# Optimization experiments

Hardware: AMD Instinct MI355X
Metric: run time of the kernel (lower is better)

## Reference

```python
import jax, jax.numpy as jnp
import numpy as np
from jax import lax

T, B, V, N = 128, 256, 256, 1024


def setup_inputs() -> dict:
    key = jax.random.key(0)
    k1, k2, k3, k4 = jax.random.split(key, 4)
    inputs = jax.random.uniform(k1, (T, B, V), dtype=jnp.float32)
    labels = jax.random.uniform(k2, (T * B, V), dtype=jnp.float32)
    weights = jax.random.normal(k3, (V + N, N), dtype=jnp.float32) * 0.1
    bias = jnp.zeros((N,), dtype=jnp.float32)
    output_weights = jax.random.normal(k4, (N, V), dtype=jnp.float32) * 0.1
    output_bias = jnp.zeros((V,), dtype=jnp.float32)
    return {
        "inputs": inputs,
        "labels": labels,
        "weights": weights,
        "bias": bias,
        "output_weights": output_weights,
        "output_bias": output_bias,
    }


def reference(inputs, labels, weights, bias, output_weights, output_bias):
    t, b, v = inputs.shape
    n = weights.shape[1]
    # split concat-matmul into x@Wx + h@Wh (same math as concat([x,h]) @ W)
    w_x = weights[:v]   # [V, N]
    w_h = weights[v:]   # [N, N]

    def step(h, x):
        h_new = jnp.tanh(x @ w_x + h @ w_h + bias)
        return h_new, h_new

    h0 = jnp.zeros((b, n), dtype=inputs.dtype)
    _, outputs = lax.scan(step, h0, inputs)          # [T, B, N]
    outputs = outputs.reshape(t * b, n)              # concat over time
    logits = outputs @ output_weights + output_bias  # [T*B, V]
    # softmax_cross_entropy_with_logits (soft labels), then mean
    log_p = jax.nn.log_softmax(logits, axis=-1)
    loss = jnp.mean(-jnp.sum(labels * log_p, axis=-1))
    return loss
```

## Files before the change

### kernel.cpp

```cpp
#include <hip/hip_runtime.h>
#include <math.h>

typedef __bf16 bf16;
typedef __attribute__((ext_vector_type(4))) __bf16 bf16x4;
typedef __attribute__((ext_vector_type(8))) __bf16 bf16x8;
typedef __attribute__((ext_vector_type(4))) float f32x4;

#define T_STEPS 128
#define B_SZ    256
#define V_SZ    256
#define N_SZ    1024
#define NROWS   (T_STEPS * B_SZ)
#define RSTR    68
#define LSTR    17
#define NGRP    16
#define NCB     16

__device__ __forceinline__ float fast_tanh(float x) {
    float e = __expf(2.0f * x);
    return 1.0f - 2.0f / (e + 1.0f);
}

__device__ __forceinline__ bf16x8 cvt_bf16x8(float4 a, float4 b) {
    bf16x8 r;
    r[0] = (bf16)a.x; r[1] = (bf16)a.y; r[2] = (bf16)a.z; r[3] = (bf16)a.w;
    r[4] = (bf16)b.x; r[5] = (bf16)b.y; r[6] = (bf16)b.z; r[7] = (bf16)b.w;
    return r;
}

__global__ __launch_bounds__(256) void k_prep(
    const float* __restrict__ weights,
    const float* __restrict__ out_w,
    bf16* __restrict__ Wxt,
    bf16* __restrict__ Wht,
    bf16* __restrict__ Wot)
{
    __shared__ float tile[32][33];
    int id = blockIdx.x;
    const float* src; bf16* dst; int R, C, tr, tc;
    if (id < 256) {
        src = weights; dst = Wxt; R = V_SZ; C = N_SZ;
        tr = (id & 7) * 32; tc = (id >> 3) * 32;
    } else if (id < 1280) {
        id -= 256;
        src = weights + (size_t)V_SZ * N_SZ; dst = Wht; R = N_SZ; C = N_SZ;
        tr = (id & 31) * 32; tc = (id >> 5) * 32;
    } else {
        id -= 1280;
        src = out_w; dst = Wot; R = N_SZ; C = V_SZ;
        tr = (id & 31) * 32; tc = (id >> 5) * 32;
    }
    int tx = threadIdx.x & 31;
    int ty = threadIdx.x >> 5;
#pragma unroll
    for (int i = 0; i < 32; i += 8)
        tile[ty + i][tx] = src[(size_t)(tr + ty + i) * C + tc + tx];
    __syncthreads();
#pragma unroll
    for (int i = 0; i < 32; i += 8)
        dst[(size_t)(tc + ty + i) * R + tr + tx] = (bf16)tile[tx][ty + i];
}

__global__ __launch_bounds__(512, 2) void k_rnn(
    const float* __restrict__ Xf,
    const bf16* __restrict__ Wxt,
    const bf16* __restrict__ Wht,
    const bf16* __restrict__ Wot,
    const float* __restrict__ bias,
    bf16* __restrict__ XH,
    unsigned int* __restrict__ Lgu,
    int* __restrict__ cnt)
{
    __shared__ float red[8 * 16 * RSTR];
    __shared__ float lred[8 * 16 * LSTR];
    const int tid  = threadIdx.x;
    const int lane = tid & 63;
    const int w    = tid >> 6;
    const int quad = lane >> 4;
    const int l15  = lane & 15;
    const int g  = blockIdx.x >> 4;
    const int c  = blockIdx.x & 15;
    const int m0 = g * 16;
    const int n0 = c * 64;
    const int k0 = w * 128;
    const int v0 = w * 32;
    int* gcnt = cnt + g * T_STEPS;

    const bf16* Bp = Wht + (size_t)(n0 + l15) * N_SZ + k0 + quad * 8;
    bf16x8 b[4][4];
#pragma unroll
    for (int nt = 0; nt < 4; ++nt)
#pragma unroll
        for (int kc = 0; kc < 4; ++kc)
            b[nt][kc] = *(const bf16x8*)&Bp[(size_t)(nt * 16) * N_SZ + kc * 32];
    bf16x8 bx[4];
#pragma unroll
    for (int nt = 0; nt < 4; ++nt)
        bx[nt] = *(const bf16x8*)&Wxt[(size_t)(n0 + nt * 16 + l15) * V_SZ + v0 + quad * 8];
    bf16x8 bo[4];
#pragma unroll
    for (int kc = 0; kc < 4; ++kc)
        bo[kc] = *(const bf16x8*)&Wot[(size_t)(c * 16 + l15) * N_SZ + k0 + kc * 32 + quad * 8];

    const int orow = tid >> 5;
    const int ocol = (tid & 31) * 2;
    const float bias0 = bias[n0 + ocol];
    const float bias1 = bias[n0 + ocol + 1];
    const int lrow = w * 2 + (lane >> 3);
    const int lvp  = lane & 7;
    unsigned int* XHu = (unsigned int*)XH;
    const f32x4 zz = {0.f, 0.f, 0.f, 0.f};
    const size_t xin = (size_t)(m0 + l15) * V_SZ + v0 + quad * 8;

    {
        float4 f0 = *(const float4*)&Xf[xin];
        float4 f1 = *(const float4*)&Xf[xin + 4];
        bf16x8 ax = cvt_bf16x8(f0, f1);
        f32x4 acc[4] = {zz, zz, zz, zz};
#pragma unroll
        for (int nt = 0; nt < 4; ++nt)
            acc[nt] = __builtin_amdgcn_mfma_f32_16x16x32_bf16(ax, bx[nt], acc[nt], 0, 0, 0);
#pragma unroll
        for (int nt = 0; nt < 4; ++nt)
#pragma unroll
            for (int r = 0; r < 4; ++r)
                red[(w * 16 + quad * 4 + r) * RSTR + nt * 16 + l15] = acc[nt][r];
        __syncthreads();
        float s0 = bias0, s1 = bias1;
#pragma unroll
        for (int w2 = 0; w2 < 8; ++w2) {
            float2 v = *(const float2*)&red[(w2 * 16 + orow) * RSTR + ocol];
            s0 += v.x; s1 += v.y;
        }
        bf16 r0 = (bf16)fast_tanh(s0);
        bf16 r1 = (bf16)fast_tanh(s1);
        unsigned int outw = (unsigned int)__builtin_bit_cast(unsigned short, r0)
                          | ((unsigned int)__builtin_bit_cast(unsigned short, r1) << 16);
        size_t oidx = (((size_t)m0 + orow) * N_SZ + n0 + ocol) >> 1;
        __hip_atomic_store(&XHu[oidx], outw, __ATOMIC_RELAXED, __HIP_MEMORY_SCOPE_AGENT);
        asm volatile("s_waitcnt vmcnt(0)" ::: "memory");
        __syncthreads();
        if (tid == 0)
            __hip_atomic_fetch_add(&gcnt[0], 1, __ATOMIC_RELAXED, __HIP_MEMORY_SCOPE_AGENT);
    }

    for (int t = 1; t < T_STEPS; ++t) {
        float4 f0 = *(const float4*)&Xf[(size_t)t * B_SZ * V_SZ + xin];
        float4 f1 = *(const float4*)&Xf[(size_t)t * B_SZ * V_SZ + xin + 4];

        if (tid == 0) {
            while (__hip_atomic_load(&gcnt[t - 1], __ATOMIC_RELAXED,
                                     __HIP_MEMORY_SCOPE_AGENT) < NCB)
                __builtin_amdgcn_s_sleep(1);
        }
        __syncthreads();

        const bf16* Ap = XH + ((size_t)(t - 1) * B_SZ + m0 + l15) * N_SZ + k0 + quad * 8;
        bf16x8 a[4];
#pragma unroll
        for (int kc = 0; kc < 4; ++kc)
            a[kc] = *(const bf16x8*)&Ap[kc * 32];

        bf16x8 ax = cvt_bf16x8(f0, f1);
        f32x4 acc[4] = {zz, zz, zz, zz};
#pragma unroll
        for (int nt = 0; nt < 4; ++nt)
            acc[nt] = __builtin_amdgcn_mfma_f32_16x16x32_bf16(ax, bx[nt], acc[nt], 0, 0, 0);
#pragma unroll
        for (int kc = 0; kc < 4; ++kc)
#pragma unroll
            for (int nt = 0; nt < 4; ++nt)
                acc[nt] = __builtin_amdgcn_mfma_f32_16x16x32_bf16(a[kc], b[nt][kc],
                                                                  acc[nt], 0, 0, 0);
        f32x4 lacc = zz;
#pragma unroll
        for (int kc = 0; kc < 4; ++kc)
            lacc = __builtin_amdgcn_mfma_f32_16x16x32_bf16(a[kc], bo[kc], lacc, 0, 0, 0);

#pragma unroll
        for (int nt = 0; nt < 4; ++nt)
#pragma unroll
            for (int r = 0; r < 4; ++r)
                red[(w * 16 + quad * 4 + r) * RSTR + nt * 16 + l15] = acc[nt][r];
#pragma unroll
        for (int r = 0; r < 4; ++r)
            lred[(w * 16 + quad * 4 + r) * LSTR + l15] = lacc[r];
        __syncthreads();

        float s0 = bias0, s1 = bias1;
#pragma unroll
        for (int w2 = 0; w2 < 8; ++w2) {
            float2 v = *(const float2*)&red[(w2 * 16 + orow) * RSTR + ocol];
            s0 += v.x; s1 += v.y;
        }
        bf16 r0 = (bf16)fast_tanh(s0);
        bf16 r1 = (bf16)fast_tanh(s1);
        unsigned int outw = (unsigned int)__builtin_bit_cast(unsigned short, r0)
                          | ((unsigned int)__builtin_bit_cast(unsigned short, r1) << 16);
        size_t oidx = (((size_t)t * B_SZ + m0 + orow) * N_SZ + n0 + ocol) >> 1;
        __hip_atomic_store(&XHu[oidx], outw, __ATOMIC_RELAXED, __HIP_MEMORY_SCOPE_AGENT);

        if (lane < 16) {
            float sa = 0.f, sb = 0.f;
#pragma unroll
            for (int w2 = 0; w2 < 8; ++w2) {
                sa += lred[(w2 * 16 + lrow) * LSTR + lvp * 2];
                sb += lred[(w2 * 16 + lrow) * LSTR + lvp * 2 + 1];
            }
            bf16 pa = (bf16)sa, pb = (bf16)sb;
            unsigned int pw = (unsigned int)__builtin_bit_cast(unsigned short, pa)
                            | ((unsigned int)__builtin_bit_cast(unsigned short, pb) << 16);
            Lgu[(((size_t)(t - 1) * 16 + c) * B_SZ + m0 + lrow) * 8 + lvp] = pw;
        }

        asm volatile("s_waitcnt vmcnt(0)" ::: "memory");
        __syncthreads();
        if (tid == 0)
            __hip_atomic_fetch_add(&gcnt[t], 1, __ATOMIC_RELAXED, __HIP_MEMORY_SCOPE_AGENT);
    }

    if (tid == 0) {
        while (__hip_atomic_load(&gcnt[T_STEPS - 1], __ATOMIC_RELAXED,
                                 __HIP_MEMORY_SCOPE_AGENT) < NCB)
            __builtin_amdgcn_s_sleep(1);
    }
    __syncthreads();
    {
        const bf16* Ap = XH + ((size_t)(T_STEPS - 1) * B_SZ + m0 + l15) * N_SZ + k0 + quad * 8;
        bf16x8 a[4];
#pragma unroll
        for (int kc = 0; kc < 4; ++kc)
            a[kc] = *(const bf16x8*)&Ap[kc * 32];
        f32x4 lacc = zz;
#pragma unroll
        for (int kc = 0; kc < 4; ++kc)
            lacc = __builtin_amdgcn_mfma_f32_16x16x32_bf16(a[kc], bo[kc], lacc, 0, 0, 0);
#pragma unroll
        for (int r = 0; r < 4; ++r)
            lred[(w * 16 + quad * 4 + r) * LSTR + l15] = lacc[r];
        __syncthreads();
        if (lane < 16) {
            float sa = 0.f, sb = 0.f;
#pragma unroll
            for (int w2 = 0; w2 < 8; ++w2) {
                sa += lred[(w2 * 16 + lrow) * LSTR + lvp * 2];
                sb += lred[(w2 * 16 + lrow) * LSTR + lvp * 2 + 1];
            }
            bf16 pa = (bf16)sa, pb = (bf16)sb;
            unsigned int pw = (unsigned int)__builtin_bit_cast(unsigned short, pa)
                            | ((unsigned int)__builtin_bit_cast(unsigned short, pb) << 16);
            Lgu[(((size_t)(T_STEPS - 1) * 16 + c) * B_SZ + m0 + lrow) * 8 + lvp] = pw;
        }
    }
}

__global__ __launch_bounds__(256) void k_lred(
    const bf16* __restrict__ Lg,
    const float* __restrict__ labels,
    const float* __restrict__ ob,
    float* __restrict__ out)
{
    __shared__ float bt[4];
    const int tid  = threadIdx.x;
    const int lane = tid & 63;
    const int w    = tid >> 6;
    const int cs   = lane >> 2;
    const int vi   = (lane & 3) * 4;
    const float4 ob4 = *(const float4*)&ob[cs * 16 + vi];

    float wtot = 0.f;
    for (int i = 0; i < 32; ++i) {
        int row  = blockIdx.x * 128 + w * 32 + i;
        int p    = row >> 8;
        int brow = row & 255;
        bf16x4 lv = *(const bf16x4*)&Lg[(((size_t)p * 16 + cs) * B_SZ + brow) * 16 + vi];
        float l0 = (float)lv.x + ob4.x;
        float l1 = (float)lv.y + ob4.y;
        float l2 = (float)lv.z + ob4.z;
        float l3 = (float)lv.w + ob4.w;
        float mx = fmaxf(fmaxf(l0, l1), fmaxf(l2, l3));
#pragma unroll
        for (int sft = 1; sft < 64; sft <<= 1)
            mx = fmaxf(mx, __shfl_xor(mx, sft, 64));
        float sume = __expf(l0 - mx) + __expf(l1 - mx) + __expf(l2 - mx) + __expf(l3 - mx);
        const float4 lb = *(const float4*)&labels[(size_t)row * V_SZ + cs * 16 + vi];
        float labs = lb.x + lb.y + lb.z + lb.w;
        float labv = lb.x * l0 + lb.y * l1 + lb.z * l2 + lb.w * l3;
#pragma unroll
        for (int sft = 1; sft < 64; sft <<= 1) {
            sume += __shfl_xor(sume, sft, 64);
            labs += __shfl_xor(labs, sft, 64);
            labv += __shfl_xor(labv, sft, 64);
        }
        float lse = mx + __logf(sume);
        wtot += labs * lse - labv;
    }
    if (lane == 0) bt[w] = wtot;
    __syncthreads();
    if (tid == 0)
        atomicAdd(out, (bt[0] + bt[1] + bt[2] + bt[3]) * (1.0f / (float)NROWS));
}

extern "C" void kernel_launch(void* const* d_in, const int* in_sizes, int n_in,
                              void* d_out, int out_size, void* d_ws, size_t ws_size,
                              hipStream_t stream)
{
    const float* inputs  = (const float*)d_in[0];
    const float* labels  = (const float*)d_in[1];
    const float* weights = (const float*)d_in[2];
    const float* bias    = (const float*)d_in[3];
    const float* out_w   = (const float*)d_in[4];
    const float* out_b   = (const float*)d_in[5];
    float* out = (float*)d_out;

    char* ws = (char*)d_ws;
    bf16* XH  = (bf16*)ws;  ws += (size_t)NROWS * N_SZ * 2;
    bf16* Lg  = (bf16*)ws;  ws += (size_t)NROWS * V_SZ * 2;
    bf16* Wxt = (bf16*)ws;  ws += (size_t)N_SZ * V_SZ * 2;
    bf16* Wht = (bf16*)ws;  ws += (size_t)N_SZ * N_SZ * 2;
    bf16* Wot = (bf16*)ws;  ws += (size_t)V_SZ * N_SZ * 2;
    int*  cnt = (int*)ws;   ws += (size_t)NGRP * T_STEPS * 4;

    hipMemsetAsync(out, 0, sizeof(float), stream);
    hipMemsetAsync(cnt, 0, (size_t)NGRP * T_STEPS * 4, stream);

    k_prep<<<dim3(1536), 256, 0, stream>>>(weights, out_w, Wxt, Wht, Wot);

    k_rnn<<<dim3(NGRP * NCB), 512, 0, stream>>>(inputs, Wxt, Wht, Wot, bias, XH,
                                                (unsigned int*)Lg, cnt);

    k_lred<<<dim3(NROWS / 128), 256, 0, stream>>>(Lg, labels, out_b, out);
}
```

Measured before the change: 503.1 us.

## Replace per-step group counter with per-block flags and per-wave waits

Each block now sets its own per-step ready flag instead of incrementing a shared counter. Each wave polls only the two producer blocks whose hidden-state columns it reads, so the block-wide barrier after the wait is gone. The x-projection MFMAs are moved ahead of the wait, and the logits MFMA and reduction are moved after the flag publish, so the recurrence critical path is shorter. The cost is 16x more flag memory, many more poll loads, and an extra barrier around the logits reduction.

```diff
diff --git a/kernel.cpp b/kernel.cpp
--- a/kernel.cpp
+++ b/kernel.cpp
@@ -69,7 +69,7 @@
     const float* __restrict__ bias,
     bf16* __restrict__ XH,
     unsigned int* __restrict__ Lgu,
-    int* __restrict__ cnt)
+    int* __restrict__ flg)
 {
     __shared__ float red[8 * 16 * RSTR];
     __shared__ float lred[8 * 16 * LSTR];
@@ -84,7 +84,9 @@
     const int n0 = c * 64;
     const int k0 = w * 128;
     const int v0 = w * 32;
-    int* gcnt = cnt + g * T_STEPS;
+    int* gflg  = flg + g * (NCB * T_STEPS);
+    int* myflg = gflg + c * T_STEPS;
+    int* pflg  = gflg + (2 * w + (lane & 1)) * T_STEPS;
 
     const bf16* Bp = Wht + (size_t)(n0 + l15) * N_SZ + k0 + quad * 8;
     bf16x8 b[4][4];
@@ -141,19 +143,24 @@
         asm volatile("s_waitcnt vmcnt(0)" ::: "memory");
         __syncthreads();
         if (tid == 0)
-            __hip_atomic_fetch_add(&gcnt[0], 1, __ATOMIC_RELAXED, __HIP_MEMORY_SCOPE_AGENT);
+            __hip_atomic_store(&myflg[0], 1, __ATOMIC_RELAXED, __HIP_MEMORY_SCOPE_AGENT);
     }
 
     for (int t = 1; t < T_STEPS; ++t) {
         float4 f0 = *(const float4*)&Xf[(size_t)t * B_SZ * V_SZ + xin];
         float4 f1 = *(const float4*)&Xf[(size_t)t * B_SZ * V_SZ + xin + 4];
-
-        if (tid == 0) {
-            while (__hip_atomic_load(&gcnt[t - 1], __ATOMIC_RELAXED,
-                                     __HIP_MEMORY_SCOPE_AGENT) < NCB)
+        bf16x8 ax = cvt_bf16x8(f0, f1);
+        f32x4 acc[4] = {zz, zz, zz, zz};
+#pragma unroll
+        for (int nt = 0; nt < 4; ++nt)
+            acc[nt] = __builtin_amdgcn_mfma_f32_16x16x32_bf16(ax, bx[nt], acc[nt], 0, 0, 0);
+
+        if (lane < 2) {
+            while (__hip_atomic_load(&pflg[t - 1], __ATOMIC_RELAXED,
+                                     __HIP_MEMORY_SCOPE_AGENT) == 0)
                 __builtin_amdgcn_s_sleep(1);
         }
-        __syncthreads();
+        asm volatile("" ::: "memory");
 
         const bf16* Ap = XH + ((size_t)(t - 1) * B_SZ + m0 + l15) * N_SZ + k0 + quad * 8;
         bf16x8 a[4];
@@ -161,30 +168,17 @@
         for (int kc = 0; kc < 4; ++kc)
             a[kc] = *(const bf16x8*)&Ap[kc * 32];
 
-        bf16x8 ax = cvt_bf16x8(f0, f1);
-        f32x4 acc[4] = {zz, zz, zz, zz};
-#pragma unroll
-        for (int nt = 0; nt < 4; ++nt)
-            acc[nt] = __builtin_amdgcn_mfma_f32_16x16x32_bf16(ax, bx[nt], acc[nt], 0, 0, 0);
 #pragma unroll
         for (int kc = 0; kc < 4; ++kc)
 #pragma unroll
             for (int nt = 0; nt < 4; ++nt)
                 acc[nt] = __builtin_amdgcn_mfma_f32_16x16x32_bf16(a[kc], b[nt][kc],
                                                                   acc[nt], 0, 0, 0);
-        f32x4 lacc = zz;
-#pragma unroll
-        for (int kc = 0; kc < 4; ++kc)
-            lacc = __builtin_amdgcn_mfma_f32_16x16x32_bf16(a[kc], bo[kc], lacc, 0, 0, 0);
-
 #pragma unroll
         for (int nt = 0; nt < 4; ++nt)
 #pragma unroll
             for (int r = 0; r < 4; ++r)
                 red[(w * 16 + quad * 4 + r) * RSTR + nt * 16 + l15] = acc[nt][r];
-#pragma unroll
-        for (int r = 0; r < 4; ++r)
-            lred[(w * 16 + quad * 4 + r) * LSTR + l15] = lacc[r];
         __syncthreads();
 
         float s0 = bias0, s1 = bias1;
@@ -200,6 +194,19 @@
         size_t oidx = (((size_t)t * B_SZ + m0 + orow) * N_SZ + n0 + ocol) >> 1;
         __hip_atomic_store(&XHu[oidx], outw, __ATOMIC_RELAXED, __HIP_MEMORY_SCOPE_AGENT);
 
+        asm volatile("s_waitcnt vmcnt(0)" ::: "memory");
+        __syncthreads();
+        if (tid == 0)
+            __hip_atomic_store(&myflg[t], 1, __ATOMIC_RELAXED, __HIP_MEMORY_SCOPE_AGENT);
+
+        f32x4 lacc = zz;
+#pragma unroll
+        for (int kc = 0; kc < 4; ++kc)
+            lacc = __builtin_amdgcn_mfma_f32_16x16x32_bf16(a[kc], bo[kc], lacc, 0, 0, 0);
+#pragma unroll
+        for (int r = 0; r < 4; ++r)
+            lred[(w * 16 + quad * 4 + r) * LSTR + l15] = lacc[r];
+        __syncthreads();
         if (lane < 16) {
             float sa = 0.f, sb = 0.f;
 #pragma unroll
@@ -212,19 +219,14 @@
                             | ((unsigned int)__builtin_bit_cast(unsigned short, pb) << 16);
             Lgu[(((size_t)(t - 1) * 16 + c) * B_SZ + m0 + lrow) * 8 + lvp] = pw;
         }
-
-        asm volatile("s_waitcnt vmcnt(0)" ::: "memory");
-        __syncthreads();
-        if (tid == 0)
-            __hip_atomic_fetch_add(&gcnt[t], 1, __ATOMIC_RELAXED, __HIP_MEMORY_SCOPE_AGENT);
-    }
-
-    if (tid == 0) {
-        while (__hip_atomic_load(&gcnt[T_STEPS - 1], __ATOMIC_RELAXED,
-                                 __HIP_MEMORY_SCOPE_AGENT) < NCB)
+    }
+
+    if (lane < 2) {
+        while (__hip_atomic_load(&pflg[T_STEPS - 1], __ATOMIC_RELAXED,
+                                 __HIP_MEMORY_SCOPE_AGENT) == 0)
             __builtin_amdgcn_s_sleep(1);
     }
-    __syncthreads();
+    asm volatile("" ::: "memory");
     {
         const bf16* Ap = XH + ((size_t)(T_STEPS - 1) * B_SZ + m0 + l15) * N_SZ + k0 + quad * 8;
         bf16x8 a[4];
@@ -235,6 +237,7 @@
 #pragma unroll
         for (int kc = 0; kc < 4; ++kc)
             lacc = __builtin_amdgcn_mfma_f32_16x16x32_bf16(a[kc], bo[kc], lacc, 0, 0, 0);
+        __syncthreads();
 #pragma unroll
         for (int r = 0; r < 4; ++r)
             lred[(w * 16 + quad * 4 + r) * LSTR + l15] = lacc[r];
@@ -319,15 +322,15 @@
     bf16* Wxt = (bf16*)ws;  ws += (size_t)N_SZ * V_SZ * 2;
     bf16* Wht = (bf16*)ws;  ws += (size_t)N_SZ * N_SZ * 2;
     bf16* Wot = (bf16*)ws;  ws += (size_t)V_SZ * N_SZ * 2;
-    int*  cnt = (int*)ws;   ws += (size_t)NGRP * T_STEPS * 4;
+    int*  flg = (int*)ws;   ws += (size_t)NGRP * NCB * T_STEPS * 4;
 
     hipMemsetAsync(out, 0, sizeof(float), stream);
-    hipMemsetAsync(cnt, 0, (size_t)NGRP * T_STEPS * 4, stream);
+    hipMemsetAsync(flg, 0, (size_t)NGRP * NCB * T_STEPS * 4, stream);
 
     k_prep<<<dim3(1536), 256, 0, stream>>>(weights, out_w, Wxt, Wht, Wot);
 
     k_rnn<<<dim3(NGRP * NCB), 512, 0, stream>>>(inputs, Wxt, Wht, Wot, bias, XH,
-                                                (unsigned int*)Lg, cnt);
+                                                (unsigned int*)Lg, flg);
 
     k_lred<<<dim3(NROWS / 128), 256, 0, stream>>>(Lg, labels, out_b, out);
 }
```

New measurement: 519.4 us. 3.2% more time.
